# Kernel tuning notes

Measured on AMD Instinct MI355X. Metric: run time of the kernel, lower is better.

Reference implementation:

```python
import jax, jax.numpy as jnp
import numpy as np

B, S, HID = 2, 2048, 2048
NH, HD, RD = 16, 128, 64
KVC, QC = 512, 1536


def _apply_rope(t):
    # t: [B, H, S, R]; standard half-split rotary embedding
    R = t.shape[-1]
    s = t.shape[-2]
    inv_freq = 1.0 / (10000.0 ** (jnp.arange(0, R, 2, dtype=jnp.float32) / R))  # [R/2]
    ang = jnp.arange(s, dtype=jnp.float32)[:, None] * inv_freq[None, :]  # [S, R/2]
    cos, sin = jnp.cos(ang), jnp.sin(ang)
    t1, t2 = t[..., : R // 2], t[..., R // 2 :]
    return jnp.concatenate([t1 * cos - t2 * sin, t2 * cos + t1 * sin], axis=-1)


def setup_inputs() -> dict:
    key = jax.random.key(0)
    ks = jax.random.split(key, 20)

    def lin(k, fan_in, fan_out):
        bound = 1.0 / np.sqrt(fan_in)
        kw, kb = jax.random.split(k)
        W = jax.random.uniform(kw, (fan_in, fan_out), jnp.float32, -bound, bound)
        b = jax.random.uniform(kb, (fan_out,), jnp.float32, -bound, bound)
        return W, b

    x = jax.random.normal(ks[0], (B, S, HID), jnp.float32)
    W_kvd, b_kvd = lin(ks[1], HID, KVC)
    W_ku, b_ku = lin(ks[2], KVC, NH * HD)
    W_vu, b_vu = lin(ks[3], KVC, NH * HD)
    W_kr, b_kr = lin(ks[4], KVC, NH * RD)
    W_qd, b_qd = lin(ks[5], HID, QC)
    W_qu, b_qu = lin(ks[6], QC, NH * HD)
    W_qr, b_qr = lin(ks[7], QC, NH * RD)
    W_o, b_o = lin(ks[8], NH * HD, HID)
    return dict(x=x, W_kvd=W_kvd, b_kvd=b_kvd, W_ku=W_ku, b_ku=b_ku,
                W_vu=W_vu, b_vu=b_vu, W_kr=W_kr, b_kr=b_kr,
                W_qd=W_qd, b_qd=b_qd, W_qu=W_qu, b_qu=b_qu,
                W_qr=W_qr, b_qr=b_qr, W_o=W_o, b_o=b_o)


def reference(x, W_kvd, b_kvd, W_ku, b_ku, W_vu, b_vu, W_kr, b_kr,
              W_qd, b_qd, W_qu, b_qu, W_qr, b_qr, W_o, b_o):
    b, s, _ = x.shape

    def heads(t, d):  # [B,S,NH*d] -> [B,NH,S,d]
        return t.reshape(b, s, NH, d).transpose(0, 2, 1, 3)

    kv_c = x @ W_kvd + b_kvd                     # [B,S,KVC]
    keys_c = heads(kv_c @ W_ku + b_ku, HD)       # [B,H,S,HD]
    values = heads(kv_c @ W_vu + b_vu, HD)
    keys_r = _apply_rope(heads(kv_c @ W_kr + b_kr, RD))

    q_c = x @ W_qd + b_qd                        # [B,S,QC]
    queries_c = heads(q_c @ W_qu + b_qu, HD)
    queries_r = _apply_rope(heads(q_c @ W_qr + b_qr, RD))

    q = jnp.concatenate([queries_c, queries_r], axis=-1)  # [B,H,S,HD+RD]
    k = jnp.concatenate([keys_c, keys_r], axis=-1)

    scale = 1.0 / np.sqrt(HD + RD)
    scores = jnp.einsum('bhqd,bhkd->bhqk', q, k) * scale
    causal = jnp.triu(jnp.ones((s, s), dtype=bool), k=1)
    scores = jnp.where(causal[None, None], jnp.float32(-1e9), scores)
    probs = jax.nn.softmax(scores, axis=-1)
    ctx = jnp.einsum('bhqk,bhkd->bhqd', probs, values)    # [B,H,S,HD]
    ctx = ctx.transpose(0, 2, 1, 3).reshape(b, s, NH * HD)
    return ctx @ W_o + b_o
```

## Files before the change

### kernel.cpp

```cpp
#include <hip/hip_runtime.h>
#include <math.h>

#define BB   2
#define SS   2048
#define HIDD 2048
#define NHH  16
#define HDD  128
#define RDD  64
#define KVCC 512
#define QCC  1536
#define DQK  192
#define MROWS 4096

using bf16x8 = __attribute__((ext_vector_type(8))) short;
using short4v = __attribute__((ext_vector_type(4))) short;
using f32x4  = __attribute__((ext_vector_type(4))) float;
using f32x16 = __attribute__((ext_vector_type(16))) float;

static __device__ __forceinline__ float b2f(short s) {
    unsigned u = ((unsigned)(unsigned short)s) << 16;
    union { unsigned u; float f; } v; v.u = u; return v.f;
}
static __device__ __forceinline__ short f2b(float f) {
    union { float f; unsigned u; } v; v.f = f;
    unsigned r = (v.u + 0x7fffu + ((v.u >> 16) & 1u)) >> 16;
    return (short)r;
}
static __device__ __forceinline__ unsigned cvtpk(float lo, float hi) {
    unsigned r;
    asm("v_cvt_pk_bf16_f32 %0, %1, %2" : "=v"(r) : "v"(lo), "v"(hi));
    return r;
}

#define GLOAD16(gsrc, ldst) \
    __builtin_amdgcn_global_load_lds((const __attribute__((address_space(1))) void*)(gsrc), \
                                     (__attribute__((address_space(3))) void*)(ldst), 16, 0, 0)

__global__ void cvt_kernel(const float* __restrict__ in, short* __restrict__ out) {
    int i = (blockIdx.x * blockDim.x + threadIdx.x) * 4;
    float4 v = *(const float4*)(in + i);
    short4v o;
    o[0] = f2b(v.x); o[1] = f2b(v.y); o[2] = f2b(v.z); o[3] = f2b(v.w);
    *(short4v*)(out + i) = o;
}

__global__ void wtrans_kernel(
    const float* __restrict__ W0, const float* __restrict__ W1,
    const float* __restrict__ W2, const float* __restrict__ W3,
    const float* __restrict__ W4, const float* __restrict__ W5,
    const float* __restrict__ W6, const float* __restrict__ W7,
    short* __restrict__ D0, short* __restrict__ D1,
    short* __restrict__ D2, short* __restrict__ D3) {
    __shared__ float t[32][33];
    int bid = blockIdx.x;
    const float* W; short* Dst; int K, N, lt;
    if (bid < 4096) {
        if (bid < 1024) { W = W0; Dst = D0;                        K = 2048; N = 512;  lt = bid; }
        else            { W = W1; Dst = D0 + (size_t)512 * 2048;   K = 2048; N = 1536; lt = bid - 1024; }
    } else if (bid < 6656) {
        if (bid < 5120)      { W = W2; Dst = D1;                       K = 512; N = 2048; lt = bid - 4096; }
        else if (bid < 6144) { W = W3; Dst = D1 + (size_t)2048 * 512;  K = 512; N = 2048; lt = bid - 5120; }
        else                 { W = W4; Dst = D1 + (size_t)4096 * 512;  K = 512; N = 1024; lt = bid - 6144; }
    } else if (bid < 11264) {
        if (bid < 9728) { W = W5; Dst = D2;                        K = 1536; N = 2048; lt = bid - 6656; }
        else            { W = W6; Dst = D2 + (size_t)2048 * 1536;  K = 1536; N = 1024; lt = bid - 9728; }
    } else { W = W7; Dst = D3; K = 2048; N = 2048; lt = bid - 11264; }
    int ntx = N >> 5;
    int n0 = (lt % ntx) * 32, k0 = (lt / ntx) * 32;
    int tx = threadIdx.x, ty = threadIdx.y;
#pragma unroll
    for (int i = 0; i < 4; i++)
        t[ty + i * 8][tx] = W[(size_t)(k0 + ty + i * 8) * N + n0 + tx];
    __syncthreads();
#pragma unroll
    for (int i = 0; i < 4; i++)
        Dst[(size_t)(n0 + ty + i * 8) * K + k0 + tx] = f2b(t[tx][ty + i * 8]);
}

template <int ID>
__global__ __launch_bounds__(256) void gemm128(
    const short* __restrict__ A, const short* __restrict__ Bt,
    const float* __restrict__ b0, const float* __restrict__ b1, const float* __restrict__ b2,
    void* __restrict__ C0, void* __restrict__ C1,
    int M, int N, int K) {
    __shared__ short Asm[3][4096];
    __shared__ short Bsm[3][4096];
    int tid = threadIdx.x, lane = tid & 63, w = tid >> 6;
    int wm = w >> 1, wn = w & 1;
    int m0 = blockIdx.y * 128, n0 = blockIdx.x * 128;
    int fr = lane & 15, fk = (lane >> 4) * 8;
    const short* Ag = A + (size_t)(m0 + (tid >> 2)) * K + (tid & 3) * 8;
    const short* Bg = Bt + (size_t)(n0 + (tid >> 2)) * K + (tid & 3) * 8;
    auto stage = [&](int t, int b) {
        int k0 = t * 32;
        GLOAD16(Ag + k0, &Asm[b][tid * 8]);
        GLOAD16(Ag + k0 + (size_t)64 * K, &Asm[b][2048 + tid * 8]);
        GLOAD16(Bg + k0, &Bsm[b][tid * 8]);
        GLOAD16(Bg + k0 + (size_t)64 * K, &Bsm[b][2048 + tid * 8]);
    };
    f32x4 acc[4][4] = {};
    int NT = K >> 5;
    stage(0, 0);
    stage(1, 1);
    for (int t = 0; t < NT; t++) {
        int cur = t % 3;
        if (t + 1 < NT) asm volatile("s_waitcnt vmcnt(4)" ::: "memory");
        else            asm volatile("s_waitcnt vmcnt(0)" ::: "memory");
        __builtin_amdgcn_s_barrier();
        bf16x8 af[4], bfv[4];
#pragma unroll
        for (int m = 0; m < 4; m++)
            af[m] = *(const bf16x8*)&Asm[cur][(wm * 64 + m * 16 + fr) * 32 + fk];
#pragma unroll
        for (int n = 0; n < 4; n++)
            bfv[n] = *(const bf16x8*)&Bsm[cur][(wn * 64 + n * 16 + fr) * 32 + fk];
#pragma unroll
        for (int m = 0; m < 4; m++)
#pragma unroll
            for (int n = 0; n < 4; n++)
                acc[m][n] = __builtin_amdgcn_mfma_f32_16x16x32_bf16(af[m], bfv[n], acc[m][n], 0, 0, 0);
        __builtin_amdgcn_s_barrier();
        if (t + 2 < NT) stage(t + 2, (t + 2) % 3);
    }
#pragma unroll
    for (int m = 0; m < 4; m++)
#pragma unroll
        for (int n = 0; n < 4; n++)
#pragma unroll
            for (int r = 0; r < 4; r++) {
                int row = m0 + wm * 64 + m * 16 + ((lane >> 4) << 2) + r;
                int col = n0 + wn * 64 + n * 16 + fr;
                float v = acc[m][n][r];
                if constexpr (ID == 0) {
                    ((float*)C0)[(size_t)row * N + col] = v + b0[col];
                } else if constexpr (ID == 1) {
                    if (col < KVCC)
                        ((short*)C0)[(size_t)row * KVCC + col] = f2b(v + b0[col]);
                    else
                        ((short*)C1)[(size_t)row * QCC + (col - KVCC)] = f2b(v + b1[col - KVCC]);
                } else if constexpr (ID == 2) {
                    int b = row >> 11, s = row & (SS - 1);
                    if (col < 2048) {
                        int h = col >> 7, d = col & 127;
                        ((short*)C0)[(((size_t)(b * NHH + h)) * SS + s) * DQK + d] = f2b(v + b0[col]);
                    } else if (col < 4096) {
                        int c = col - 2048; int h = c >> 7, d = c & 127;
                        ((short*)C1)[(((size_t)(b * NHH + h)) * HDD + d) * SS + s] = f2b(v + b1[c]);
                    } else {
                        int c = col - 4096; int h = c >> 6, d = c & 63;
                        ((short*)C0)[(((size_t)(b * NHH + h)) * SS + s) * DQK + HDD + d] = f2b(v + b2[c]);
                    }
                } else {
                    int b = row >> 11, s = row & (SS - 1);
                    if (col < 2048) {
                        int h = col >> 7, d = col & 127;
                        ((short*)C0)[(((size_t)(b * NHH + h)) * SS + s) * DQK + d] = f2b(v + b0[col]);
                    } else {
                        int c = col - 2048; int h = c >> 6, d = c & 63;
                        ((short*)C0)[(((size_t)(b * NHH + h)) * SS + s) * DQK + HDD + d] = f2b(v + b1[c]);
                    }
                }
            }
}

__global__ void rope_kernel(short* __restrict__ Tk, short* __restrict__ Tq) {
    int idx = blockIdx.x * blockDim.x + threadIdx.x;
    const int HALF = BB * NHH * SS * 32;
    short* T = (idx < HALF) ? Tk : Tq;
    int id = (idx < HALF) ? idx : idx - HALF;
    int i = id & 31;
    int s = (id >> 5) & (SS - 1);
    int bh = id >> 16;
    short* p = T + ((size_t)bh * SS + s) * DQK + HDD;
    float t1 = b2f(p[i]), t2 = b2f(p[i + 32]);
    float inv = exp2f(-(float)i * 0.41524101186092034f);
    float ang = (float)s * inv;
    float sn, cs;
    sincosf(ang, &sn, &cs);
    p[i] = f2b(t1 * cs - t2 * sn);
    p[i + 32] = f2b(t2 * cs + t1 * sn);
}

__global__ __launch_bounds__(256, 2) void attn_kernel(
    const short* __restrict__ Q, const short* __restrict__ Kg,
    const short* __restrict__ Vt, short* __restrict__ ctx) {
    __shared__ short Ksm[2][64 * 192];
    __shared__ short Vsm[2][128 * 64];
    int tid = threadIdx.x, lane = tid & 63, w = tid >> 6;
    int hf = lane >> 5, l31 = lane & 31;
    int bid = blockIdx.x;
    int half = bid >> 8, a = (bid & 255) >> 5;
    int qt = half ? a : 15 - a;
    int bh = bid & 31;
    int bb = bh >> 4, hd = bh & 15;
    int q0 = qt * 128;
    const short* Qp = Q + (size_t)bh * SS * DQK;
    const short* Kp = Kg + (size_t)bh * SS * DQK;
    const char*  Vp = (const char*)(Vt + (size_t)bh * HDD * SS);
    int wr0 = q0 + w * 32;
    int qrow = wr0 + l31;
    const float scale = 0.07216878364870323f;
    const float L2E = 1.44269504088896f;

    bf16x8 qf[12];
#pragma unroll
    for (int s = 0; s < 12; s++)
        qf[s] = *(const bf16x8*)(Qp + (size_t)qrow * DQK + s * 16 + hf * 8);

    f32x16 acc[4] = {};
    float mrow = -1e30f, lsum = 0.f;
    int nt = 2 * qt + 2;

    auto stageK = [&](int key0, int b) {
#pragma unroll
        for (int pp = 0; pp < 6; pp++) {
            int flat = pp * 4096 + tid * 16;
            int row = flat / 384, bir = flat - row * 384;
            const char* src = (const char*)Kp + (size_t)(key0 + row) * 384 + (bir ^ ((row & 7) << 4));
            GLOAD16(src, (char*)Ksm[b] + flat);
        }
    };
    auto stageV = [&](int key0, int b) {
#pragma unroll
        for (int c = 0; c < 4; c++) {
            int flat = c * 4096 + tid * 16;
            int d = flat >> 7, bik = flat & 127;
            const char* src = Vp + (size_t)d * (SS * 2) + (size_t)key0 * 2 + (bik ^ ((d & 7) << 4));
            GLOAD16(src, (char*)Vsm[b] + flat);
        }
    };

    stageK(0, 0); stageV(0, 0);
    __syncthreads();

    for (int t0 = 0; t0 < nt; t0++) {
        int key0 = t0 * 64;
        int cur = t0 & 1;
        if (t0 + 1 < nt) { stageK(key0 + 64, cur ^ 1); stageV(key0 + 64, cur ^ 1); }
        bool active = (key0 <= wr0 + 31);
        if (active) {
            f32x16 z = {};
            f32x16 sv0 = z, sv1 = z;
            int xr = (l31 & 7) << 4;
            const char* Kb = (const char*)Ksm[cur];
            __builtin_amdgcn_s_setprio(1);
#pragma unroll
            for (int s = 0; s < 12; s++) {
                bf16x8 k0 = *(const bf16x8*)(Kb + l31 * 384 + ((s * 32 + hf * 16) ^ xr));
                bf16x8 k1 = *(const bf16x8*)(Kb + (32 + l31) * 384 + ((s * 32 + hf * 16) ^ xr));
                sv0 = __builtin_amdgcn_mfma_f32_32x32x16_bf16(k0, qf[s], sv0, 0, 0, 0);
                sv1 = __builtin_amdgcn_mfma_f32_32x32x16_bf16(k1, qf[s], sv1, 0, 0, 0);
            }
            __builtin_amdgcn_s_setprio(0);
            bool domask = (key0 + 63 > wr0);
            float p[32];
#pragma unroll
            for (int t = 0; t < 2; t++)
#pragma unroll
                for (int r = 0; r < 16; r++) {
                    float v = (t ? sv1[r] : sv0[r]);
                    int key = key0 + 32 * t + (r & 3) + 8 * (r >> 2) + 4 * hf;
                    if (domask && key > qrow) v = -1e30f;
                    p[t * 16 + r] = v;
                }
            float tm[16];
#pragma unroll
            for (int i = 0; i < 16; i++) tm[i] = fmaxf(p[i], p[i + 16]);
#pragma unroll
            for (int i = 0; i < 8; i++) tm[i] = fmaxf(tm[i], tm[i + 8]);
#pragma unroll
            for (int i = 0; i < 4; i++) tm[i] = fmaxf(tm[i], tm[i + 4]);
            float pmaxs = fmaxf(fmaxf(tm[0], tm[1]), fmaxf(tm[2], tm[3])) * scale;
            if (__any(pmaxs > mrow + 8.f)) {
                float pc = fmaxf(pmaxs, __shfl_xor(pmaxs, 32, 64));
                float mn = fmaxf(mrow, pc);
                float al = exp2f((mrow - mn) * L2E);
                mrow = mn;
                lsum *= al;
                float arl[16];
#pragma unroll
                for (int r = 0; r < 16; r++)
                    arl[r] = __shfl(al, (r & 3) + 8 * (r >> 2) + 4 * hf, 64);
#pragma unroll
                for (int n = 0; n < 4; n++)
#pragma unroll
                    for (int r = 0; r < 16; r++)
                        acc[n][r] *= arl[r];
            }
            float sL = scale * L2E, mL = mrow * L2E;
#pragma unroll
            for (int i = 0; i < 32; i++)
                p[i] = exp2f(fmaf(p[i], sL, -mL));
            float ts[16];
#pragma unroll
            for (int i = 0; i < 16; i++) ts[i] = p[i] + p[i + 16];
#pragma unroll
            for (int i = 0; i < 8; i++) ts[i] = ts[i] + ts[i + 8];
#pragma unroll
            for (int i = 0; i < 4; i++) ts[i] = ts[i] + ts[i + 4];
            lsum += (ts[0] + ts[1]) + (ts[2] + ts[3]);
            bf16x8 afv[4];
#pragma unroll
            for (int g = 0; g < 4; g++) {
                int base = (g >> 1) * 16 + (g & 1) * 8;
                unsigned a01 = cvtpk(p[base + 0], p[base + 1]);
                unsigned a23 = cvtpk(p[base + 2], p[base + 3]);
                unsigned b01 = cvtpk(p[base + 4], p[base + 5]);
                unsigned b23 = cvtpk(p[base + 6], p[base + 7]);
                unsigned s0 = hf ? a01 : b01, s1 = hf ? a23 : b23;
                unsigned r0 = (unsigned)__shfl_xor((int)s0, 32, 64);
                unsigned r1 = (unsigned)__shfl_xor((int)s1, 32, 64);
                union { unsigned u[4]; bf16x8 v; } af;
                af.u[0] = hf ? r0 : a01;
                af.u[1] = hf ? r1 : a23;
                af.u[2] = hf ? b01 : r0;
                af.u[3] = hf ? b23 : r1;
                afv[g] = af.v;
            }
            const char* Vb = (const char*)Vsm[cur];
            __builtin_amdgcn_s_setprio(1);
#pragma unroll
            for (int g = 0; g < 4; g++)
#pragma unroll
                for (int n = 0; n < 4; n++) {
                    int d = n * 32 + l31;
                    bf16x8 vf = *(const bf16x8*)(Vb + d * 128 + ((g * 32 + hf * 16) ^ ((d & 7) << 4)));
                    acc[n] = __builtin_amdgcn_mfma_f32_32x32x16_bf16(afv[g], vf, acc[n], 0, 0, 0);
                }
            __builtin_amdgcn_s_setprio(0);
        }
        __syncthreads();
    }
    lsum += __shfl_xor(lsum, 32, 64);
    float rc = 1.0f / lsum;
    float rcl[16];
#pragma unroll
    for (int r = 0; r < 16; r++)
        rcl[r] = __shfl(rc, (r & 3) + 8 * (r >> 2) + 4 * hf, 64);
#pragma unroll
    for (int n = 0; n < 4; n++)
#pragma unroll
        for (int r = 0; r < 16; r++) {
            int row = wr0 + (r & 3) + 8 * (r >> 2) + 4 * hf;
            int d = n * 32 + l31;
            ctx[((size_t)(bb * SS + row)) * (NHH * HDD) + hd * HDD + d] = f2b(acc[n][r] * rcl[r]);
        }
}

extern "C" void kernel_launch(void* const* d_in, const int* in_sizes, int n_in,
                              void* d_out, int out_size, void* d_ws, size_t ws_size,
                              hipStream_t stream) {
    const float* x     = (const float*)d_in[0];
    const float* W_kvd = (const float*)d_in[1];  const float* b_kvd = (const float*)d_in[2];
    const float* W_ku  = (const float*)d_in[3];  const float* b_ku  = (const float*)d_in[4];
    const float* W_vu  = (const float*)d_in[5];  const float* b_vu  = (const float*)d_in[6];
    const float* W_kr  = (const float*)d_in[7];  const float* b_kr  = (const float*)d_in[8];
    const float* W_qd  = (const float*)d_in[9];  const float* b_qd  = (const float*)d_in[10];
    const float* W_qu  = (const float*)d_in[11]; const float* b_qu  = (const float*)d_in[12];
    const float* W_qr  = (const float*)d_in[13]; const float* b_qr  = (const float*)d_in[14];
    const float* W_o   = (const float*)d_in[15]; const float* b_o   = (const float*)d_in[16];
    float* out = (float*)d_out;

    char* p = (char*)d_ws;
    auto alloc = [&](size_t elems) {
        short* r = (short*)p;
        p += ((elems * 2) + 255) & ~(size_t)255;
        return r;
    };
    short* xb   = alloc((size_t)MROWS * HIDD);
    short* kvc  = alloc((size_t)MROWS * KVCC);
    short* qc   = alloc((size_t)MROWS * QCC);
    short* kbuf = alloc((size_t)BB * NHH * SS * DQK);
    short* qbuf = alloc((size_t)BB * NHH * SS * DQK);
    short* vtb  = alloc((size_t)BB * NHH * HDD * SS);
    short* ctx  = alloc((size_t)MROWS * NHH * HDD);
    short* Wt1  = alloc((size_t)2048 * 2048);
    short* Wt2  = alloc((size_t)5120 * 512);
    short* Wt3  = alloc((size_t)3072 * 1536);
    short* Wt4  = alloc((size_t)2048 * 2048);

    cvt_kernel<<<dim3((MROWS * HIDD) / 1024), dim3(256), 0, stream>>>(x, xb);
    dim3 tb(32, 8);
    wtrans_kernel<<<dim3(15360), tb, 0, stream>>>(
        W_kvd, W_qd, W_ku, W_vu, W_kr, W_qu, W_qr, W_o, Wt1, Wt2, Wt3, Wt4);

    gemm128<1><<<dim3(2048 / 128, MROWS / 128), 256, 0, stream>>>(
        xb, Wt1, b_kvd, b_qd, nullptr, kvc, qc, MROWS, 2048, 2048);
    gemm128<2><<<dim3(5120 / 128, MROWS / 128), 256, 0, stream>>>(
        kvc, Wt2, b_ku, b_vu, b_kr, kbuf, vtb, MROWS, 5120, 512);
    gemm128<3><<<dim3(3072 / 128, MROWS / 128), 256, 0, stream>>>(
        qc, Wt3, b_qu, b_qr, nullptr, qbuf, nullptr, MROWS, 3072, 1536);

    rope_kernel<<<dim3((2 * BB * NHH * SS * 32) / 256), dim3(256), 0, stream>>>(kbuf, qbuf);

    attn_kernel<<<dim3(512), 256, 0, stream>>>(qbuf, kbuf, vtb, ctx);

    gemm128<0><<<dim3(HIDD / 128, MROWS / 128), 256, 0, stream>>>(
        ctx, Wt4, b_o, nullptr, nullptr, out, nullptr, MROWS, HIDD, NHH * HDD);
}
```

Baseline: 387.8 us.

## Merge K/V and Q up-projection GEMMs into one launch with XCD-aware block swizzle

Fuses the two up-projection GEMMs (kv_c→K/V/Kr and q_c→Q/Qr) into a single kernel that interleaves their tiles 5:3 within groups of eight. It also remaps block IDs so consecutive tiles land on the same XCD, for better L2 reuse across all GEMMs. The merged launch removes one kernel boundary and lets the short-K and long-K tiles share the device. In exchange, the blocks are imbalanced (K=512 vs K=1536) and the grid is now 1D with a swizzle that assumes the grid size divides by 8.

Result: no change. 389.2 us (+0.4%).

```diff
diff --git a/kernel.cpp b/kernel.cpp
--- a/kernel.cpp
+++ b/kernel.cpp
@@ -80,14 +80,17 @@
 template <int ID>
 __global__ __launch_bounds__(256) void gemm128(
     const short* __restrict__ A, const short* __restrict__ Bt,
-    const float* __restrict__ b0, const float* __restrict__ b1, const float* __restrict__ b2,
+    const float* __restrict__ b0, const float* __restrict__ b1,
     void* __restrict__ C0, void* __restrict__ C1,
     int M, int N, int K) {
     __shared__ short Asm[3][4096];
     __shared__ short Bsm[3][4096];
     int tid = threadIdx.x, lane = tid & 63, w = tid >> 6;
     int wm = w >> 1, wn = w & 1;
-    int m0 = blockIdx.y * 128, n0 = blockIdx.x * 128;
+    int nbx = N >> 7;
+    int cpx = gridDim.x >> 3;
+    int swz = ((int)blockIdx.x & 7) * cpx + ((int)blockIdx.x >> 3);
+    int m0 = (swz / nbx) * 128, n0 = (swz % nbx) * 128;
     int fr = lane & 15, fk = (lane >> 4) * 8;
     const short* Ag = A + (size_t)(m0 + (tid >> 2)) * K + (tid & 3) * 8;
     const short* Bg = Bt + (size_t)(n0 + (tid >> 2)) * K + (tid & 3) * 8;
@@ -133,31 +136,95 @@
                 float v = acc[m][n][r];
                 if constexpr (ID == 0) {
                     ((float*)C0)[(size_t)row * N + col] = v + b0[col];
-                } else if constexpr (ID == 1) {
+                } else {
                     if (col < KVCC)
                         ((short*)C0)[(size_t)row * KVCC + col] = f2b(v + b0[col]);
                     else
                         ((short*)C1)[(size_t)row * QCC + (col - KVCC)] = f2b(v + b1[col - KVCC]);
-                } else if constexpr (ID == 2) {
-                    int b = row >> 11, s = row & (SS - 1);
+                }
+            }
+}
+
+__global__ __launch_bounds__(256) void gemm23_kernel(
+    const short* __restrict__ kvc, const short* __restrict__ qc,
+    const short* __restrict__ Wt2, const short* __restrict__ Wt3,
+    const float* __restrict__ b_ku, const float* __restrict__ b_vu, const float* __restrict__ b_kr,
+    const float* __restrict__ b_qu, const float* __restrict__ b_qr,
+    short* __restrict__ kbuf, short* __restrict__ qbuf, short* __restrict__ vtb) {
+    __shared__ short Asm[3][4096];
+    __shared__ short Bsm[3][4096];
+    int tid = threadIdx.x, lane = tid & 63, w = tid >> 6;
+    int wm = w >> 1, wn = w & 1;
+    int cpx = gridDim.x >> 3;
+    int swz = ((int)blockIdx.x & 7) * cpx + ((int)blockIdx.x >> 3);
+    int g = swz >> 3, rm = swz & 7;
+    bool is3 = rm < 3;
+    const short *A, *Bt; int K, nbx, lid;
+    if (is3) { A = qc;  Bt = Wt3; K = 1536; nbx = 3072 / 128; lid = g * 3 + rm; }
+    else     { A = kvc; Bt = Wt2; K = 512;  nbx = 5120 / 128; lid = g * 5 + (rm - 3); }
+    int m0 = (lid / nbx) * 128, n0 = (lid % nbx) * 128;
+    int fr = lane & 15, fk = (lane >> 4) * 8;
+    const short* Ag = A + (size_t)(m0 + (tid >> 2)) * K + (tid & 3) * 8;
+    const short* Bg = Bt + (size_t)(n0 + (tid >> 2)) * K + (tid & 3) * 8;
+    auto stage = [&](int t, int b) {
+        int k0 = t * 32;
+        GLOAD16(Ag + k0, &Asm[b][tid * 8]);
+        GLOAD16(Ag + k0 + (size_t)64 * K, &Asm[b][2048 + tid * 8]);
+        GLOAD16(Bg + k0, &Bsm[b][tid * 8]);
+        GLOAD16(Bg + k0 + (size_t)64 * K, &Bsm[b][2048 + tid * 8]);
+    };
+    f32x4 acc[4][4] = {};
+    int NT = K >> 5;
+    stage(0, 0);
+    stage(1, 1);
+    for (int t = 0; t < NT; t++) {
+        int cur = t % 3;
+        if (t + 1 < NT) asm volatile("s_waitcnt vmcnt(4)" ::: "memory");
+        else            asm volatile("s_waitcnt vmcnt(0)" ::: "memory");
+        __builtin_amdgcn_s_barrier();
+        bf16x8 af[4], bfv[4];
+#pragma unroll
+        for (int m = 0; m < 4; m++)
+            af[m] = *(const bf16x8*)&Asm[cur][(wm * 64 + m * 16 + fr) * 32 + fk];
+#pragma unroll
+        for (int n = 0; n < 4; n++)
+            bfv[n] = *(const bf16x8*)&Bsm[cur][(wn * 64 + n * 16 + fr) * 32 + fk];
+#pragma unroll
+        for (int m = 0; m < 4; m++)
+#pragma unroll
+            for (int n = 0; n < 4; n++)
+                acc[m][n] = __builtin_amdgcn_mfma_f32_16x16x32_bf16(af[m], bfv[n], acc[m][n], 0, 0, 0);
+        __builtin_amdgcn_s_barrier();
+        if (t + 2 < NT) stage(t + 2, (t + 2) % 3);
+    }
+#pragma unroll
+    for (int m = 0; m < 4; m++)
+#pragma unroll
+        for (int n = 0; n < 4; n++)
+#pragma unroll
+            for (int r = 0; r < 4; r++) {
+                int row = m0 + wm * 64 + m * 16 + ((lane >> 4) << 2) + r;
+                int col = n0 + wn * 64 + n * 16 + fr;
+                float v = acc[m][n][r];
+                int b = row >> 11, s = row & (SS - 1);
+                if (is3) {
                     if (col < 2048) {
                         int h = col >> 7, d = col & 127;
-                        ((short*)C0)[(((size_t)(b * NHH + h)) * SS + s) * DQK + d] = f2b(v + b0[col]);
+                        qbuf[(((size_t)(b * NHH + h)) * SS + s) * DQK + d] = f2b(v + b_qu[col]);
+                    } else {
+                        int c = col - 2048; int h = c >> 6, d = c & 63;
+                        qbuf[(((size_t)(b * NHH + h)) * SS + s) * DQK + HDD + d] = f2b(v + b_qr[c]);
+                    }
+                } else {
+                    if (col < 2048) {
+                        int h = col >> 7, d = col & 127;
+                        kbuf[(((size_t)(b * NHH + h)) * SS + s) * DQK + d] = f2b(v + b_ku[col]);
                     } else if (col < 4096) {
                         int c = col - 2048; int h = c >> 7, d = c & 127;
-                        ((short*)C1)[(((size_t)(b * NHH + h)) * HDD + d) * SS + s] = f2b(v + b1[c]);
+                        vtb[(((size_t)(b * NHH + h)) * HDD + d) * SS + s] = f2b(v + b_vu[c]);
                     } else {
                         int c = col - 4096; int h = c >> 6, d = c & 63;
-                        ((short*)C0)[(((size_t)(b * NHH + h)) * SS + s) * DQK + HDD + d] = f2b(v + b2[c]);
-                    }
-                } else {
-                    int b = row >> 11, s = row & (SS - 1);
-                    if (col < 2048) {
-                        int h = col >> 7, d = col & 127;
-                        ((short*)C0)[(((size_t)(b * NHH + h)) * SS + s) * DQK + d] = f2b(v + b0[col]);
-                    } else {
-                        int c = col - 2048; int h = c >> 6, d = c & 63;
-                        ((short*)C0)[(((size_t)(b * NHH + h)) * SS + s) * DQK + HDD + d] = f2b(v + b1[c]);
+                        kbuf[(((size_t)(b * NHH + h)) * SS + s) * DQK + HDD + d] = f2b(v + b_kr[c]);
                     }
                 }
             }
@@ -384,17 +451,15 @@
     wtrans_kernel<<<dim3(15360), tb, 0, stream>>>(
         W_kvd, W_qd, W_ku, W_vu, W_kr, W_qu, W_qr, W_o, Wt1, Wt2, Wt3, Wt4);
 
-    gemm128<1><<<dim3(2048 / 128, MROWS / 128), 256, 0, stream>>>(
-        xb, Wt1, b_kvd, b_qd, nullptr, kvc, qc, MROWS, 2048, 2048);
-    gemm128<2><<<dim3(5120 / 128, MROWS / 128), 256, 0, stream>>>(
-        kvc, Wt2, b_ku, b_vu, b_kr, kbuf, vtb, MROWS, 5120, 512);
-    gemm128<3><<<dim3(3072 / 128, MROWS / 128), 256, 0, stream>>>(
-        qc, Wt3, b_qu, b_qr, nullptr, qbuf, nullptr, MROWS, 3072, 1536);
+    gemm128<1><<<dim3(512), 256, 0, stream>>>(
+        xb, Wt1, b_kvd, b_qd, kvc, qc, MROWS, 2048, 2048);
+    gemm23_kernel<<<dim3(2048), 256, 0, stream>>>(
+        kvc, qc, Wt2, Wt3, b_ku, b_vu, b_kr, b_qu, b_qr, kbuf, qbuf, vtb);
 
     rope_kernel<<<dim3((2 * BB * NHH * SS * 32) / 256), dim3(256), 0, stream>>>(kbuf, qbuf);
 
     attn_kernel<<<dim3(512), 256, 0, stream>>>(qbuf, kbuf, vtb, ctx);
 
-    gemm128<0><<<dim3(HIDD / 128, MROWS / 128), 256, 0, stream>>>(
-        ctx, Wt4, b_o, nullptr, nullptr, out, nullptr, MROWS, HIDD, NHH * HDD);
-}
+    gemm128<0><<<dim3(512), 256, 0, stream>>>(
+        ctx, Wt4, b_o, nullptr, out, nullptr, MROWS, HIDD, NHH * HDD);
+}
```
